# Kernel optimization log

Measured on AMD Instinct MI355X. Metric: run time of the kernel, lower is better.

## Reference

```python
import jax, jax.numpy as jnp
import numpy as np

NUM_HEADS = 8
N_MOD = 3


def _sinusoidal_pe(seq_len, d_model):
    # standard sinusoidal table [seq_len, d_model]
    pos = np.arange(seq_len, dtype=np.float32)[:, None]
    div = np.exp(np.arange(0, d_model, 2, dtype=np.float32) * (-np.log(10000.0) / d_model))
    pe = np.zeros((seq_len, d_model), dtype=np.float32)
    pe[:, 0::2] = np.sin(pos * div)
    pe[:, 1::2] = np.cos(pos * div)
    return jnp.asarray(pe)


def _attn_mask(dim_x, dim_z, n_mod):
    # additive mask [dim_x, dim_x + n_mod*dim_z]: 0 where allowed, -inf elsewhere
    blocks = [np.eye(dim_x, dtype=np.float32)]
    for _ in range(n_mod):  # all modalities present (mod_list == full_mod)
        p2 = np.zeros((dim_x, dim_z), dtype=np.float32)
        p2[dim_x - dim_z:, :] = np.eye(dim_z, dtype=np.float32)
        blocks.append(p2)
    m = np.concatenate(blocks, axis=1)
    return jnp.asarray(np.where(m < 1, -np.inf, 0.0).astype(np.float32))


def setup_inputs() -> dict:
    key = jax.random.key(0)
    ks = jax.random.split(key, 8)
    bs, en, dx, dz = 32, 256, 512, 256
    state = jax.random.normal(ks[0], (bs, en, dx), jnp.float32)
    obs0 = jax.random.normal(ks[1], (bs, en, dz), jnp.float32)
    obs1 = jax.random.normal(ks[2], (bs, en, dz), jnp.float32)
    obs2 = jax.random.normal(ks[3], (bs, en, dz), jnp.float32)
    Q = jax.random.uniform(ks[4], (dx, en), jnp.float32)  # torch.rand init
    Wq = jax.random.normal(ks[5], (en, en), jnp.float32) / np.sqrt(en)
    Wk = jax.random.normal(ks[6], (en, en), jnp.float32) / np.sqrt(en)
    bq = jnp.zeros((en,), jnp.float32)
    bk = jnp.zeros((en,), jnp.float32)
    return {"state": state, "obs0": obs0, "obs1": obs1, "obs2": obs2,
            "Q": Q, "Wq": Wq, "bq": bq, "Wk": Wk, "bk": bk}


def reference(state, obs0, obs1, obs2, Q, Wq, bq, Wk, bk):
    bs, en, dx = state.shape
    dz = obs0.shape[2]
    obs_list = (obs0, obs1, obs2)
    mask = _attn_mask(dx, dz, N_MOD)            # [dx, L]
    pe = _sinusoidal_pe(bs, en)                 # positions run over batch axis (faithful quirk)

    # mean-center over the ensemble axis
    A = state - jnp.mean(state, axis=1, keepdims=True)          # [bs, en, dx]
    Ys = [o - jnp.mean(o, axis=1, keepdims=True) for o in obs_list]

    # build query / key-value sequences in [tokens, bs, en] layout, add PE, then batch-major
    q = Q[:, None, :] + pe[None, :, :]                          # [dx, bs, en]
    xy = jnp.concatenate([jnp.transpose(A, (2, 0, 1))]
                         + [jnp.transpose(Y, (2, 0, 1)) for Y in Ys], axis=0)
    xy = xy + pe[None, :, :]                                    # [L, bs, en]
    qb = jnp.transpose(q, (1, 0, 2))                            # [bs, dx, en]
    kb = jnp.transpose(xy, (1, 0, 2))                           # [bs, L, en]

    # multi-head masked attention (output path is discarded by the original module,
    # only the attention map is used, so no V/O projection is needed)
    dh = en // NUM_HEADS
    qh = (qb @ Wq + bq).reshape(bs, dx, NUM_HEADS, dh).transpose(0, 2, 1, 3)   # [bs,h,dx,dh]
    kh = (kb @ Wk + bk).reshape(bs, -1, NUM_HEADS, dh).transpose(0, 2, 1, 3)   # [bs,h,L,dh]
    scores = jnp.einsum('bhqd,bhkd->bhqk', qh, kh) / np.sqrt(dh).astype(np.float32)
    scores = scores + mask[None, None, :, :]
    atten = jnp.mean(jax.nn.softmax(scores, axis=-1), axis=1)   # [bs, dx, L]

    # attn-weighted matmul over concatenated raw state+obs
    merge = jnp.concatenate([state, obs0, obs1, obs2], axis=2)  # [bs, en, L]
    new_state = jnp.einsum('bql,bel->beq', atten, merge)        # [bs, en, dx]
    return new_state, atten
```

## Files before the change

kernel.cpp:

```cpp
#include <hip/hip_runtime.h>
#include <math.h>


__global__ void k_uv(const float* __restrict__ Q, const float* __restrict__ Wq,
                     const float* __restrict__ bq,
                     float* __restrict__ u, float* __restrict__ v) {
  __shared__ float row[256];
  const int f = threadIdx.x;
  const int blk = blockIdx.x;
  float rv;
  if (blk < 256) {
    rv = Q[(256 + blk) * 256 + f];
  } else {
    const int b = blk - 256;
    const float dv = expf(-9.210340371976184f * (float)((f >> 1) << 1) * (1.0f / 256.0f));
    const float ang = (float)b * dv;
    rv = (f & 1) ? cosf(ang) : sinf(ang);
  }
  row[f] = rv;
  __syncthreads();
  float acc = (blk < 256) ? 0.0f : bq[f];
  for (int e = 0; e < 256; ++e) acc += row[e] * Wq[e * 256 + f];
  if (blk < 256) u[blk * 256 + f] = acc;
  else           v[(blk - 256) * 256 + f] = acc;
}

__global__ void k_w(const float* __restrict__ Wk, const float* __restrict__ u,
                    const float* __restrict__ v, float* __restrict__ wu2,
                    float* __restrict__ wv) {
  __shared__ float wrow[256];
  const int e = blockIdx.x;
  const int t = threadIdx.x;
  wrow[t] = Wk[e * 256 + t];
  __syncthreads();
  if (blockIdx.y == 0) {
    const float* ur = u + t * 256;
#pragma unroll
    for (int h = 0; h < 8; ++h) {
      float acc = 0.0f;
#pragma unroll
      for (int d = 0; d < 32; ++d) acc += ur[h * 32 + d] * wrow[h * 32 + d];
      wu2[(h * 256 + e) * 256 + t] = acc;
    }
  } else if (t < 32) {
    const float* vr = v + t * 256;
#pragma unroll
    for (int h = 0; h < 8; ++h) {
      float acc = 0.0f;
#pragma unroll
      for (int d = 0; d < 32; ++d) acc += vr[h * 32 + d] * wrow[h * 32 + d];
      wv[(t * 8 + h) * 256 + e] = acc;
    }
  }
}

__global__ __launch_bounds__(512)
void k_mega(const float* __restrict__ state, const float* __restrict__ o0,
            const float* __restrict__ o1, const float* __restrict__ o2,
            const float* __restrict__ wu2, const float* __restrict__ wv,
            float* __restrict__ out0, float* __restrict__ out1) {
  const int blk = blockIdx.x;
  const int t = threadIdx.x;

  if (blk < 512) {
    const int jt = blk & 15;
    const int b  = blk >> 4;
    __shared__ float s_wv[2048];
    __shared__ float s_part[8][16][25];
    __shared__ float s_a[16][4];

    for (int i = t; i < 2048; i += 512) s_wv[i] = wv[b * 2048 + i];
    __syncthreads();

    const int jl = t & 15;
    const int es = (t >> 4) & 15;
    const int hp = t >> 8;
    const int j = jt * 16 + jl;

    float acc[24];
#pragma unroll
    for (int k = 0; k < 24; ++k) acc[k] = 0.f;

    const float* ps = state + (size_t)b * 256 * 512 + 256 + j;
    const float* p0 = o0 + (size_t)b * 256 * 256 + j;
    const float* p1 = o1 + (size_t)b * 256 * 256 + j;
    const float* p2 = o2 + (size_t)b * 256 * 256 + j;
    const float* pwu = wu2 + (size_t)hp * 4 * 256 * 256 + j;
    const float* pwv = s_wv + hp * 4 * 256;

#pragma unroll
    for (int it = 0; it < 16; ++it) {
      const int e = es * 16 + it;
      const float s  = ps[(size_t)e * 512];
      const float x0 = p0[(size_t)e * 256];
      const float x1 = p1[(size_t)e * 256];
      const float x2 = p2[(size_t)e * 256];
      acc[20] += s; acc[21] += x0; acc[22] += x1; acc[23] += x2;
#pragma unroll
      for (int hh = 0; hh < 4; ++hh) {
        const float w = pwu[(size_t)(hh * 256 + e) * 256] + pwv[hh * 256 + e];
        acc[hh * 5 + 0] += s * w;  acc[hh * 5 + 1] += x0 * w;
        acc[hh * 5 + 2] += x1 * w; acc[hh * 5 + 3] += x2 * w;
        acc[hh * 5 + 4] += w;
      }
    }

#pragma unroll
    for (int k = 0; k < 24; ++k) {
      acc[k] += __shfl_xor(acc[k], 16);
      acc[k] += __shfl_xor(acc[k], 32);
    }
    if ((t & 48) == 0) {
      const int w = t >> 6;
      float* p = &s_part[w][jl][0];
#pragma unroll
      for (int k = 0; k < 24; ++k) p[k] = acc[k];
    }
    __syncthreads();

    if (t < 16) {
      float tot[44];
#pragma unroll
      for (int k = 0; k < 20; ++k)
        tot[k] = s_part[0][t][k] + s_part[1][t][k] + s_part[2][t][k] + s_part[3][t][k];
#pragma unroll
      for (int k = 0; k < 20; ++k)
        tot[20 + k] = s_part[4][t][k] + s_part[5][t][k] + s_part[6][t][k] + s_part[7][t][k];
#pragma unroll
      for (int c = 0; c < 4; ++c)
        tot[40 + c] = s_part[0][t][20 + c] + s_part[1][t][20 + c] +
                      s_part[2][t][20 + c] + s_part[3][t][20 + c];

      const float m0 = tot[40] * (1.f / 256.f), m1 = tot[41] * (1.f / 256.f);
      const float m2 = tot[42] * (1.f / 256.f), m3 = tot[43] * (1.f / 256.f);
      const float inv = 0.17677669529663687f;
      float am0 = 0.f, am1 = 0.f, am2 = 0.f, am3 = 0.f;
#pragma unroll
      for (int h = 0; h < 8; ++h) {
        const float dO = tot[h * 5 + 4];
        const float s0 = (tot[h * 5 + 0] - m0 * dO) * inv;
        const float s1 = (tot[h * 5 + 1] - m1 * dO) * inv;
        const float s2 = (tot[h * 5 + 2] - m2 * dO) * inv;
        const float s3 = (tot[h * 5 + 3] - m3 * dO) * inv;
        const float mx = fmaxf(fmaxf(s0, s1), fmaxf(s2, s3));
        const float e0 = expf(s0 - mx), e1 = expf(s1 - mx);
        const float e2 = expf(s2 - mx), e3 = expf(s3 - mx);
        const float r = 1.f / (e0 + e1 + e2 + e3);
        am0 += e0 * r; am1 += e1 * r; am2 += e2 * r; am3 += e3 * r;
      }
      s_a[t][0] = am0 * 0.125f; s_a[t][1] = am1 * 0.125f;
      s_a[t][2] = am2 * 0.125f; s_a[t][3] = am3 * 0.125f;
    }
    __syncthreads();

    {
      const int jl2 = t & 15;
      const int er = t >> 4;
      const float a0 = s_a[jl2][0], a1 = s_a[jl2][1];
      const float a2 = s_a[jl2][2], a3 = s_a[jl2][3];
      const int jj = jt * 16 + jl2;
#pragma unroll
      for (int k = 0; k < 8; ++k) {
        const int e = er + 32 * k;
        const size_t idxS = ((size_t)(b * 256 + e)) * 512 + 256 + jj;
        const size_t idxO = ((size_t)(b * 256 + e)) * 256 + jj;
        out0[idxS] = a0 * state[idxS] + a1 * o0[idxO] + a2 * o1[idxO] + a3 * o2[idxO];
      }
    }

    {
      const int r = t >> 5;
      const int c = t & 31;
      const int j3 = jt * 16 + r;
      const int q = 256 + j3;
      const int comp = j3 & 3;
      const int tc0 = (256 + j3) >> 2, tc1 = (512 + j3) >> 2;
      const int tc2 = (768 + j3) >> 2, tc3 = (1024 + j3) >> 2;
      const float av0 = s_a[r][0], av1 = s_a[r][1];
      const float av2 = s_a[r][2], av3 = s_a[r][3];
      float4* orow = (float4*)(out1 + ((size_t)(b * 512 + q)) * 1280);
#pragma unroll
      for (int k = 0; k < 10; ++k) {
        const int c4 = c + 32 * k;
        float4 o = make_float4(0.f, 0.f, 0.f, 0.f);
        float val = 0.f; bool hit = false;
        if (c4 == tc0)      { val = av0; hit = true; }
        else if (c4 == tc1) { val = av1; hit = true; }
        else if (c4 == tc2) { val = av2; hit = true; }
        else if (c4 == tc3) { val = av3; hit = true; }
        if (hit) {
          if (comp == 0) o.x = val; else if (comp == 1) o.y = val;
          else if (comp == 2) o.z = val; else o.w = val;
        }
        orow[c4] = o;
      }
    }
  } else if (blk < 1536) {
    const int i2 = blk - 512;
    const int b = i2 >> 5, eg = i2 & 31;
    const int row = t >> 6;
    const int col = (t & 63) << 2;
    const int e = eg * 8 + row;
    const size_t base = ((size_t)(b * 256 + e)) * 512 + col;
    *(float4*)(out0 + base) = *(const float4*)(state + base);
  } else {
    const int i3 = blk - 1536;
    const int b = i3 >> 5, qg = i3 & 31;
    if (t < 320) {
#pragma unroll
      for (int k = 0; k < 8; ++k) {
        const int q = qg * 8 + k;
        float4 o = make_float4(0.f, 0.f, 0.f, 0.f);
        if ((q >> 2) == t) {
          const int comp = q & 3;
          if (comp == 0) o.x = 1.f; else if (comp == 1) o.y = 1.f;
          else if (comp == 2) o.z = 1.f; else o.w = 1.f;
        }
        *(float4*)(out1 + ((size_t)(b * 512 + q)) * 1280 + t * 4) = o;
      }
    }
  }
}

extern "C" void kernel_launch(void* const* d_in, const int* in_sizes, int n_in,
                              void* d_out, int out_size, void* d_ws, size_t ws_size,
                              hipStream_t stream) {
  const float* state = (const float*)d_in[0];
  const float* obs0  = (const float*)d_in[1];
  const float* obs1  = (const float*)d_in[2];
  const float* obs2  = (const float*)d_in[3];
  const float* Q     = (const float*)d_in[4];
  const float* Wq    = (const float*)d_in[5];
  const float* bq    = (const float*)d_in[6];
  const float* Wk    = (const float*)d_in[7];

  float* out0 = (float*)d_out;
  float* out1 = out0 + (size_t)32 * 256 * 512;

  float* ws  = (float*)d_ws;
  float* u   = ws;
  float* v   = u + 65536;
  float* wu2 = v + 8192;
  float* wv  = wu2 + 524288;

  k_uv<<<288, 256, 0, stream>>>(Q, Wq, bq, u, v);
  k_w<<<dim3(256, 2), 256, 0, stream>>>(Wk, u, v, wu2, wv);
  k_mega<<<2560, 512, 0, stream>>>(state, obs0, obs1, obs2, wu2, wv, out0, out1);
}
```

Before: 70.50 us.

## Split score reduction into a separate partial-sum kernel over ensemble halves

The score accumulation over the ensemble axis moves out of the mega kernel into a new k_part kernel that splits the ensemble dimension in two. This doubles the number of blocks doing the heavy reduction and halves the serial loop per thread. A second kernel, k_out, sums the two partials from workspace, computes the softmax and writes the outputs. The cost is an extra launch and a round trip of partial sums through global memory.

```diff
diff --git a/kernel.cpp b/kernel.cpp
--- a/kernel.cpp
+++ b/kernel.cpp
@@ -55,82 +55,114 @@
 }
 
 __global__ __launch_bounds__(512)
-void k_mega(const float* __restrict__ state, const float* __restrict__ o0,
+void k_part(const float* __restrict__ state, const float* __restrict__ o0,
             const float* __restrict__ o1, const float* __restrict__ o2,
             const float* __restrict__ wu2, const float* __restrict__ wv,
-            float* __restrict__ out0, float* __restrict__ out1) {
+            float* __restrict__ pws) {
+  const int t = threadIdx.x;
+  const int jl = t & 15;
+  const int es = (t >> 4) & 15;
+  const int hp = t >> 8;
+  const int jt = blockIdx.x;
+  const int eq = blockIdx.y;
+  const int b  = blockIdx.z;
+  const int j = jt * 16 + jl;
+
+  __shared__ float s_wv[1024];
+  __shared__ float s_part[8][16][25];
+
+  for (int i = t; i < 1024; i += 512)
+    s_wv[i] = wv[b * 2048 + (i >> 7) * 256 + eq * 128 + (i & 127)];
+  __syncthreads();
+
+  float acc[24];
+#pragma unroll
+  for (int k = 0; k < 24; ++k) acc[k] = 0.f;
+
+  const float* ps = state + (size_t)b * 256 * 512 + 256 + j;
+  const float* p0 = o0 + (size_t)b * 256 * 256 + j;
+  const float* p1 = o1 + (size_t)b * 256 * 256 + j;
+  const float* p2 = o2 + (size_t)b * 256 * 256 + j;
+  const float* pwu = wu2 + (size_t)hp * 4 * 256 * 256 + j;
+  const float* pwv = s_wv + hp * 4 * 128;
+
+#pragma unroll
+  for (int it = 0; it < 8; ++it) {
+    const int el = es * 8 + it;
+    const int e = eq * 128 + el;
+    const float s  = ps[(size_t)e * 512];
+    const float x0 = p0[(size_t)e * 256];
+    const float x1 = p1[(size_t)e * 256];
+    const float x2 = p2[(size_t)e * 256];
+    acc[20] += s; acc[21] += x0; acc[22] += x1; acc[23] += x2;
+#pragma unroll
+    for (int hh = 0; hh < 4; ++hh) {
+      const float w = pwu[(size_t)(hh * 256 + e) * 256] + pwv[hh * 128 + el];
+      acc[hh * 5 + 0] += s * w;  acc[hh * 5 + 1] += x0 * w;
+      acc[hh * 5 + 2] += x1 * w; acc[hh * 5 + 3] += x2 * w;
+      acc[hh * 5 + 4] += w;
+    }
+  }
+
+#pragma unroll
+  for (int k = 0; k < 24; ++k) {
+    acc[k] += __shfl_xor(acc[k], 16);
+    acc[k] += __shfl_xor(acc[k], 32);
+  }
+  if ((t & 48) == 0) {
+    const int w = t >> 6;
+    float* p = &s_part[w][jl][0];
+#pragma unroll
+    for (int k = 0; k < 24; ++k) p[k] = acc[k];
+  }
+  __syncthreads();
+
+  const size_t base = (((size_t)(jt * 32 + b)) * 2 + eq) * 704;
+  if (t < 16) {
+#pragma unroll
+    for (int k = 0; k < 20; ++k) {
+      float s = s_part[0][t][k] + s_part[1][t][k] + s_part[2][t][k] + s_part[3][t][k];
+      pws[base + k * 16 + t] = s;
+    }
+#pragma unroll
+    for (int c = 0; c < 4; ++c) {
+      float s = s_part[0][t][20 + c] + s_part[1][t][20 + c] +
+                s_part[2][t][20 + c] + s_part[3][t][20 + c];
+      pws[base + (40 + c) * 16 + t] = s;
+    }
+  } else if (t >= 256 && t < 272) {
+    const int l = t & 15;
+#pragma unroll
+    for (int k = 0; k < 20; ++k) {
+      float s = s_part[4][l][k] + s_part[5][l][k] + s_part[6][l][k] + s_part[7][l][k];
+      pws[base + (20 + k) * 16 + l] = s;
+    }
+  }
+}
+
+__global__ __launch_bounds__(512)
+void k_out(const float* __restrict__ state, const float* __restrict__ o0,
+           const float* __restrict__ o1, const float* __restrict__ o2,
+           const float* __restrict__ pws, float* __restrict__ out0,
+           float* __restrict__ out1) {
   const int blk = blockIdx.x;
   const int t = threadIdx.x;
 
   if (blk < 512) {
     const int jt = blk & 15;
     const int b  = blk >> 4;
-    __shared__ float s_wv[2048];
-    __shared__ float s_part[8][16][25];
+    __shared__ float s_tot[704];
     __shared__ float s_a[16][4];
 
-    for (int i = t; i < 2048; i += 512) s_wv[i] = wv[b * 2048 + i];
-    __syncthreads();
-
-    const int jl = t & 15;
-    const int es = (t >> 4) & 15;
-    const int hp = t >> 8;
-    const int j = jt * 16 + jl;
-
-    float acc[24];
-#pragma unroll
-    for (int k = 0; k < 24; ++k) acc[k] = 0.f;
-
-    const float* ps = state + (size_t)b * 256 * 512 + 256 + j;
-    const float* p0 = o0 + (size_t)b * 256 * 256 + j;
-    const float* p1 = o1 + (size_t)b * 256 * 256 + j;
-    const float* p2 = o2 + (size_t)b * 256 * 256 + j;
-    const float* pwu = wu2 + (size_t)hp * 4 * 256 * 256 + j;
-    const float* pwv = s_wv + hp * 4 * 256;
-
-#pragma unroll
-    for (int it = 0; it < 16; ++it) {
-      const int e = es * 16 + it;
-      const float s  = ps[(size_t)e * 512];
-      const float x0 = p0[(size_t)e * 256];
-      const float x1 = p1[(size_t)e * 256];
-      const float x2 = p2[(size_t)e * 256];
-      acc[20] += s; acc[21] += x0; acc[22] += x1; acc[23] += x2;
-#pragma unroll
-      for (int hh = 0; hh < 4; ++hh) {
-        const float w = pwu[(size_t)(hh * 256 + e) * 256] + pwv[hh * 256 + e];
-        acc[hh * 5 + 0] += s * w;  acc[hh * 5 + 1] += x0 * w;
-        acc[hh * 5 + 2] += x1 * w; acc[hh * 5 + 3] += x2 * w;
-        acc[hh * 5 + 4] += w;
-      }
-    }
-
-#pragma unroll
-    for (int k = 0; k < 24; ++k) {
-      acc[k] += __shfl_xor(acc[k], 16);
-      acc[k] += __shfl_xor(acc[k], 32);
-    }
-    if ((t & 48) == 0) {
-      const int w = t >> 6;
-      float* p = &s_part[w][jl][0];
-#pragma unroll
-      for (int k = 0; k < 24; ++k) p[k] = acc[k];
-    }
+    const size_t base = ((size_t)(jt * 32 + b)) * 1408;
+    for (int i = t; i < 704; i += 512)
+      s_tot[i] = pws[base + i] + pws[base + 704 + i];
     __syncthreads();
 
     if (t < 16) {
       float tot[44];
 #pragma unroll
-      for (int k = 0; k < 20; ++k)
-        tot[k] = s_part[0][t][k] + s_part[1][t][k] + s_part[2][t][k] + s_part[3][t][k];
-#pragma unroll
-      for (int k = 0; k < 20; ++k)
-        tot[20 + k] = s_part[4][t][k] + s_part[5][t][k] + s_part[6][t][k] + s_part[7][t][k];
-#pragma unroll
-      for (int c = 0; c < 4; ++c)
-        tot[40 + c] = s_part[0][t][20 + c] + s_part[1][t][20 + c] +
-                      s_part[2][t][20 + c] + s_part[3][t][20 + c];
-
+      for (int k = 0; k < 44; ++k) tot[k] = s_tot[k * 16 + t];
       const float m0 = tot[40] * (1.f / 256.f), m1 = tot[41] * (1.f / 256.f);
       const float m2 = tot[42] * (1.f / 256.f), m3 = tot[43] * (1.f / 256.f);
       const float inv = 0.17677669529663687f;
@@ -242,8 +274,10 @@
   float* v   = u + 65536;
   float* wu2 = v + 8192;
   float* wv  = wu2 + 524288;
+  float* pws = wv + 65536;
 
   k_uv<<<288, 256, 0, stream>>>(Q, Wq, bq, u, v);
   k_w<<<dim3(256, 2), 256, 0, stream>>>(Wk, u, v, wu2, wv);
-  k_mega<<<2560, 512, 0, stream>>>(state, obs0, obs1, obs2, wu2, wv, out0, out1);
-}
+  k_part<<<dim3(16, 2, 32), 512, 0, stream>>>(state, obs0, obs1, obs2, wu2, wv, pws);
+  k_out<<<2560, 512, 0, stream>>>(state, obs0, obs1, obs2, pws, out0, out1);
+}
```

New measurement: 72.26 us. 2.5% more time.
